# Performance work log

Measured on AMD Instinct MI355X. Metric: run time of the kernel, lower is better.

## Reference

```python
import jax, jax.numpy as jnp
import numpy as np

N_HEAD = 16


def setup_inputs() -> dict:
    key = jax.random.key(0)
    k0, k1, k2, k3 = jax.random.split(key, 4)
    b, n, d = 4, 2048, 1024
    scale = d ** -0.5
    return {
        "x": jax.random.normal(k0, (b, n, d), jnp.float32),
        "Wk": jax.random.normal(k1, (d, d), jnp.float32) * scale,
        "Wq": jax.random.normal(k2, (d, d), jnp.float32) * scale,
        "Wv": jax.random.normal(k3, (d, d), jnp.float32) * scale,
    }


def reference(x, Wk, Wq, Wv):
    b, n, d = x.shape
    hd = d // N_HEAD
    # Linear layers: y = x @ W^T (torch nn.Linear convention), no bias.
    keys = (x @ Wk.T).reshape(b, n, N_HEAD, hd).transpose(0, 2, 1, 3)     # (b,h,n,hd)
    queries = (x @ Wq.T).reshape(b, n, N_HEAD, hd).transpose(0, 2, 1, 3)  # (b,h,n,hd)
    values = (x @ Wv.T).reshape(b, n, N_HEAD, hd).transpose(0, 2, 1, 3)   # computed but UNUSED, as in source
    del values
    # Source does: attn_scores = keys @ queries.transpose(-1,-2)
    # i.e. scores[b,h,i,j] = k_i . q_j ; softmax over j (query axis); no 1/sqrt(d) scaling.
    attn_scores = jnp.einsum("bhid,bhjd->bhij", keys, queries)
    weights = jax.nn.softmax(attn_scores, axis=-1)
    # Source does: weight_scores @ keys (keys, NOT values)
    weighted = jnp.einsum("bhij,bhjd->bhid", weights, keys)  # (b,h,n,hd)
    # Source reshapes (b,h,n,hd) directly to (b,n,h*hd) WITHOUT transposing back.
    return weighted.reshape(b, n, N_HEAD * hd)
```

## Files before the change

### kernel.cpp

```cpp
#include <hip/hip_runtime.h>
#include <cstdint>
#include <cstddef>

#define NTOK 2048
#define DMODEL 1024
#define HD 64
#define MROWS 8192

using f16x8  = __attribute__((ext_vector_type(8))) _Float16;
using f16x4  = __attribute__((ext_vector_type(4))) _Float16;
using f32x4  = __attribute__((ext_vector_type(4))) float;
using f32x16 = __attribute__((ext_vector_type(16))) float;
using u16x8  = __attribute__((ext_vector_type(8))) unsigned short;
using u32x4  = __attribute__((ext_vector_type(4))) unsigned int;

#define Z16 {0.f,0.f,0.f,0.f,0.f,0.f,0.f,0.f,0.f,0.f,0.f,0.f,0.f,0.f,0.f,0.f}

__device__ __forceinline__ unsigned pkf16(float a, float b) {
  return __builtin_bit_cast(unsigned, __builtin_amdgcn_cvt_pkrtz(a, b));
}
__device__ __forceinline__ void plswap(unsigned &a, unsigned &b) {
  auto r = __builtin_amdgcn_permlane32_swap(a, b, false, false);
  a = r[0]; b = r[1];
}
__device__ __forceinline__ float fexp2(float x) {
  return __builtin_amdgcn_exp2f(x);
}

__global__ __launch_bounds__(256) void cvt_f32_f16(const float* __restrict__ in,
                                                   _Float16* __restrict__ out,
                                                   int n4, float scale) {
  int idx = blockIdx.x * 256 + threadIdx.x;
  if (idx < n4) {
    float4 v = reinterpret_cast<const float4*>(in)[idx];
    f16x4 o;
    o.x = (_Float16)(v.x * scale); o.y = (_Float16)(v.y * scale);
    o.z = (_Float16)(v.z * scale); o.w = (_Float16)(v.w * scale);
    reinterpret_cast<f16x4*>(out)[idx] = o;
  }
}

__global__ __launch_bounds__(256) void cvt_w(const float* __restrict__ Wk,
                                             const float* __restrict__ Wq,
                                             _Float16* __restrict__ Wkb,
                                             _Float16* __restrict__ Wqb) {
  const int idx = blockIdx.x * 256 + threadIdx.x;
  const float* in = blockIdx.y ? Wq : Wk;
  _Float16* out = blockIdx.y ? Wqb : Wkb;
  const float scale = blockIdx.y ? 1.4426950408889634f : 1.0f;
  float4 v = reinterpret_cast<const float4*>(in)[idx];
  f16x4 o;
  o.x = (_Float16)(v.x * scale); o.y = (_Float16)(v.y * scale);
  o.z = (_Float16)(v.z * scale); o.w = (_Float16)(v.w * scale);
  reinterpret_cast<f16x4*>(out)[idx] = o;
}

#define GLDS16(g, l) __builtin_amdgcn_global_load_lds(                      \
    (const __attribute__((address_space(1))) void*)(g),                     \
    (__attribute__((address_space(3))) void*)(l), 16, 0, 0)

__global__ __launch_bounds__(256) void gemm_f16(
    const _Float16* __restrict__ X,
    const _Float16* __restrict__ Wk,
    const _Float16* __restrict__ Wq,
    _Float16* __restrict__ Kb,
    _Float16* __restrict__ Qb) {
  const _Float16* __restrict__ W = blockIdx.z ? Wq : Wk;
  _Float16* __restrict__ Y = blockIdx.z ? Qb : Kb;

  __shared__ _Float16 As[2][128 * 32];
  __shared__ _Float16 Bs[2][128 * 32];

  const int tid = threadIdx.x;
  const int lane = tid & 63;
  const int w = tid >> 6;
  const int m0 = blockIdx.x * 128;
  const int o0 = blockIdx.y * 128;

  const int srow = w * 32 + (lane >> 2);
  const int scol = (lane & 3) * 8;
  const _Float16* xsrc = X + (size_t)(m0 + srow) * DMODEL + scol;
  const _Float16* wsrc = W + (size_t)(o0 + srow) * DMODEL + scol;

  const int wr = w >> 1, wc = w & 1;
  const int arow = lane & 15, kg = lane >> 4;

  f32x4 zero = {0.f, 0.f, 0.f, 0.f};
  f32x4 acc[4][4];
#pragma unroll
  for (int mi = 0; mi < 4; ++mi)
#pragma unroll
    for (int ni = 0; ni < 4; ++ni) acc[mi][ni] = zero;

  GLDS16(xsrc,               &As[0][(w * 32) * 32]);
  GLDS16(xsrc + 16 * DMODEL, &As[0][(w * 32 + 16) * 32]);
  GLDS16(wsrc,               &Bs[0][(w * 32) * 32]);
  GLDS16(wsrc + 16 * DMODEL, &Bs[0][(w * 32 + 16) * 32]);

  for (int kt = 0; kt < 32; ++kt) {
    __syncthreads();
    if (kt + 1 < 32) {
      const int ko = (kt + 1) * 32;
      const int bn = (kt + 1) & 1;
      GLDS16(xsrc + ko,               &As[bn][(w * 32) * 32]);
      GLDS16(xsrc + ko + 16 * DMODEL, &As[bn][(w * 32 + 16) * 32]);
      GLDS16(wsrc + ko,               &Bs[bn][(w * 32) * 32]);
      GLDS16(wsrc + ko + 16 * DMODEL, &Bs[bn][(w * 32 + 16) * 32]);
    }
    const int buf = kt & 1;
    f16x8 af[4], bfr[4];
#pragma unroll
    for (int mi = 0; mi < 4; ++mi)
      af[mi] = *reinterpret_cast<const f16x8*>(
          &As[buf][(wr * 64 + mi * 16 + arow) * 32 + kg * 8]);
#pragma unroll
    for (int ni = 0; ni < 4; ++ni)
      bfr[ni] = *reinterpret_cast<const f16x8*>(
          &Bs[buf][(wc * 64 + ni * 16 + arow) * 32 + kg * 8]);
#pragma unroll
    for (int mi = 0; mi < 4; ++mi)
#pragma unroll
      for (int ni = 0; ni < 4; ++ni)
        acc[mi][ni] = __builtin_amdgcn_mfma_f32_16x16x32_f16(
            af[mi], bfr[ni], acc[mi][ni], 0, 0, 0);
  }

#pragma unroll
  for (int mi = 0; mi < 4; ++mi) {
#pragma unroll
    for (int ni = 0; ni < 4; ++ni) {
#pragma unroll
      for (int r = 0; r < 4; ++r) {
        const int m = m0 + wr * 64 + mi * 16 + kg * 4 + r;
        const int o = o0 + wc * 64 + ni * 16 + arow;
        Y[(size_t)m * DMODEL + o] = (_Float16)acc[mi][ni][r];
      }
    }
  }
}

__global__ __launch_bounds__(256) void pack_qkt(
    const _Float16* __restrict__ Qb,
    const _Float16* __restrict__ Kb,
    _Float16* __restrict__ Qp,
    _Float16* __restrict__ KTp) {
  const int blk = blockIdx.x;
  const int bh = blk >> 5;
  const int t64 = blk & 31;
  const int b = bh >> 4, h = bh & 15;
  const int tid = threadIdx.x;
  const _Float16* Src = blockIdx.y ? Kb : Qb;

  __shared__ _Float16 t[64][72];
#pragma unroll
  for (int rr = 0; rr < 2; ++rr) {
    const int c = tid + rr * 256;
    const int jr = c >> 3, dcol = (c & 7) * 8;
    *reinterpret_cast<f16x8*>(&t[jr][dcol]) =
        *reinterpret_cast<const f16x8*>(
            &Src[(size_t)(b * NTOK + t64 * 64 + jr) * DMODEL + h * HD + dcol]);
  }
  __syncthreads();
  if (blockIdx.y == 0) {
#pragma unroll
    for (int rr = 0; rr < 2; ++rr) {
      const int cI = tid + rr * 256;
      const int rs = cI >> 8, ks = (cI >> 6) & 3, l = cI & 63;
      f16x8 v = *reinterpret_cast<const f16x8*>(
          &t[rs * 32 + (l & 31)][ks * 16 + (l >> 5) * 8]);
      const size_t ch = ((size_t)(bh * 64 + t64 * 2 + rs) * 4 + ks) * 512 + l * 8;
      *reinterpret_cast<f16x8*>(&Qp[ch]) = v;
    }
  } else {
#pragma unroll
    for (int rr = 0; rr < 2; ++rr) {
      const int cI = tid + rr * 256;
      const int ds = cI >> 8, ks = (cI >> 6) & 3, l = cI & 63;
      const int col = ds * 32 + (l & 31);
      const int row0 = ks * 16 + (l >> 5) * 8;
      f16x8 v;
#pragma unroll
      for (int e = 0; e < 8; ++e) v[e] = t[row0 + e][col];
      const size_t ch = (((size_t)(bh * 32 + t64) * 2 + ds) * 4 + ks) * 512 + l * 8;
      *reinterpret_cast<f16x8*>(&KTp[ch]) = v;
    }
  }
}

__global__ __launch_bounds__(256) void attn_mfma(
    const _Float16* __restrict__ Kb,
    const _Float16* __restrict__ Qp,
    const _Float16* __restrict__ KTp,
    float* __restrict__ out) {
  const int bid = blockIdx.x;
  const int myid = (bid & 7) * 128 + (bid >> 3);
  const int bh = myid >> 4;
  const int itile = myid & 15;
  const int b = bh >> 4, h = bh & 15;
  const int tid = threadIdx.x, lane = tid & 63, w = tid >> 6;
  const int l31 = lane & 31;
  const int hi = lane >> 5;
  const int hi8 = hi * 8;
  const int i0 = itile * 128 + w * 32;

  const _Float16* Kh   = Kb + (size_t)b * NTOK * DMODEL + h * HD;
  const _Float16* qpp  = Qp  + (size_t)bh * 131072 + lane * 8;
  const _Float16* ktpp = KTp + (size_t)bh * 131072 + lane * 8;

  __shared__ float lsl[4][32];
  __shared__ float scl[4][32];

  f16x8 kbf[4];
#pragma unroll
  for (int ks = 0; ks < 4; ++ks)
    kbf[ks] = *reinterpret_cast<const f16x8*>(
        &Kh[(size_t)(i0 + l31) * DMODEL + ks * 16 + hi8]);

  const f32x16 z16v = Z16;
  f32x16 o0 = z16v, o1 = z16v;
  float mreg = -1e30f, ls = 0.f;

  f16x8 qA0[4], qA1[4], qB0[4], qB1[4];
  f32x16 sA0, sA1, sB0, sB1;

#define LOADQ(QD0, QD1, JT)                                                   \
  _Pragma("unroll")                                                           \
  for (int ks = 0; ks < 4; ++ks) {                                            \
    QD0[ks] = *reinterpret_cast<const f16x8*>(                                \
        qpp + ((size_t)(JT) * 8 + ks) * 512);                                 \
    QD1[ks] = *reinterpret_cast<const f16x8*>(                                \
        qpp + ((size_t)(JT) * 8 + 4 + ks) * 512);                             \
  }

#define QK_TILE(SD0, SD1, Q0, Q1)                                             \
  SD0 = z16v; SD1 = z16v;                                                     \
  __builtin_amdgcn_s_setprio(1);                                              \
  _Pragma("unroll")                                                           \
  for (int ks = 0; ks < 4; ++ks) {                                            \
    SD0 = __builtin_amdgcn_mfma_f32_32x32x16_f16(Q0[ks], kbf[ks], SD0, 0,0,0);\
    SD1 = __builtin_amdgcn_mfma_f32_32x32x16_f16(Q1[ks], kbf[ks], SD1, 0,0,0);\
  }                                                                           \
  __builtin_amdgcn_s_setprio(0);

#define SMPV_TILE(S0, S1, JT)                                                 \
  {                                                                           \
          \
    f16x8 kt0[4], kt1[4];                                                     \
    _Pragma("unroll")                                                         \
    for (int ks = 0; ks < 4; ++ks) {                                          \
      kt0[ks] = *reinterpret_cast<const f16x8*>(                              \
          ktpp + ((size_t)(JT) * 8 + ks) * 512);                              \
      kt1[ks] = *reinterpret_cast<const f16x8*>(                              \
          ktpp + ((size_t)(JT) * 8 + 4 + ks) * 512);                          \
    }                                                                         \
    float m0 = fmaxf(S0[0], S1[0]);                                           \
    float m1 = fmaxf(S0[1], S1[1]);                                           \
    float m2 = fmaxf(S0[2], S1[2]);                                           \
    float m3 = fmaxf(S0[3], S1[3]);                                           \
    _Pragma("unroll")                                                         \
    for (int r = 4; r < 16; r += 4) {                                         \
      m0 = fmaxf(m0, fmaxf(S0[r], S1[r]));                                    \
      m1 = fmaxf(m1, fmaxf(S0[r + 1], S1[r + 1]));                            \
      m2 = fmaxf(m2, fmaxf(S0[r + 2], S1[r + 2]));                            \
      m3 = fmaxf(m3, fmaxf(S0[r + 3], S1[r + 3]));                            \
    }                                                                         \
    float pm = fmaxf(fmaxf(m0, m1), fmaxf(m2, m3));                           \
    pm = fmaxf(pm, __shfl_xor(pm, 32));                                       \
    if (!__all(pm <= mreg + 8.0f)) {                                          \
      const float mn = fmaxf(mreg, pm);                                       \
      const float sc = fexp2(mreg - mn);                                      \
      ls *= sc;                                                               \
      mreg = mn;                                                              \
      scl[w][l31] = sc;                                                       \
      _Pragma("unroll")                                                       \
      for (int r = 0; r < 16; ++r) {                                          \
        const int il = (r & 3) + 8 * (r >> 2) + 4 * hi;                       \
        const float scr = scl[w][il];                                         \
        o0[r] *= scr; o1[r] *= scr;                                           \
      }                                                                       \
    }                                                                         \
    float p0a[16], p1a[16];                                                   \
    _Pragma("unroll")                                                         \
    for (int r = 0; r < 16; ++r) {                                            \
      p0a[r] = fexp2(S0[r] - mreg);                                           \
      p1a[r] = fexp2(S1[r] - mreg);                                           \
    }                                                                         \
    float l0 = 0.f, l1 = 0.f, l2 = 0.f, l3 = 0.f;                             \
    _Pragma("unroll")                                                         \
    for (int r = 0; r < 16; r += 4) {                                         \
      l0 += p0a[r]     + p1a[r];                                              \
      l1 += p0a[r + 1] + p1a[r + 1];                                          \
      l2 += p0a[r + 2] + p1a[r + 2];                                          \
      l3 += p0a[r + 3] + p1a[r + 3];                                          \
    }                                                                         \
    ls += (l0 + l1) + (l2 + l3);                                              \
    f16x8 pfr[4];                                                             \
    {                                                                         \
      unsigned a0 = pkf16(p0a[0], p0a[1]),  b0 = pkf16(p0a[4], p0a[5]);       \
      unsigned a1 = pkf16(p0a[2], p0a[3]),  b1 = pkf16(p0a[6], p0a[7]);       \
      plswap(a0, b0); plswap(a1, b1);                                         \
      u32x4 t; t[0] = a0; t[1] = a1; t[2] = b0; t[3] = b1;                    \
      pfr[0] = __builtin_bit_cast(f16x8, t);                                  \
      unsigned a2 = pkf16(p0a[8], p0a[9]),   b2 = pkf16(p0a[12], p0a[13]);    \
      unsigned a3 = pkf16(p0a[10], p0a[11]), b3 = pkf16(p0a[14], p0a[15]);    \
      plswap(a2, b2); plswap(a3, b3);                                         \
      t[0] = a2; t[1] = a3; t[2] = b2; t[3] = b3;                             \
      pfr[1] = __builtin_bit_cast(f16x8, t);                                  \
      unsigned a4 = pkf16(p1a[0], p1a[1]),  b4 = pkf16(p1a[4], p1a[5]);       \
      unsigned a5 = pkf16(p1a[2], p1a[3]),  b5 = pkf16(p1a[6], p1a[7]);       \
      plswap(a4, b4); plswap(a5, b5);                                         \
      t[0] = a4; t[1] = a5; t[2] = b4; t[3] = b5;                             \
      pfr[2] = __builtin_bit_cast(f16x8, t);                                  \
      unsigned a6 = pkf16(p1a[8], p1a[9]),   b6 = pkf16(p1a[12], p1a[13]);    \
      unsigned a7 = pkf16(p1a[10], p1a[11]), b7 = pkf16(p1a[14], p1a[15]);    \
      plswap(a6, b6); plswap(a7, b7);                                         \
      t[0] = a6; t[1] = a7; t[2] = b6; t[3] = b7;                             \
      pfr[3] = __builtin_bit_cast(f16x8, t);                                  \
    }                                                                         \
    __builtin_amdgcn_s_setprio(1);                                            \
    _Pragma("unroll")                                                         \
    for (int ks = 0; ks < 4; ++ks) {                                          \
      o0 = __builtin_amdgcn_mfma_f32_32x32x16_f16(pfr[ks], kt0[ks], o0, 0,0,0);\
      o1 = __builtin_amdgcn_mfma_f32_32x32x16_f16(pfr[ks], kt1[ks], o1, 0,0,0);\
    }                                                                         \
    __builtin_amdgcn_s_setprio(0);                                            \
  }

  LOADQ(qA0, qA1, 0)
  QK_TILE(sA0, sA1, qA0, qA1)
  LOADQ(qB0, qB1, 1)

  for (int jt = 0; jt < 30; jt += 2) {
    QK_TILE(sB0, sB1, qB0, qB1)
    LOADQ(qA0, qA1, jt + 2)
    SMPV_TILE(sA0, sA1, jt)
    QK_TILE(sA0, sA1, qA0, qA1)
    LOADQ(qB0, qB1, jt + 3)
    SMPV_TILE(sB0, sB1, jt + 1)
  }
  QK_TILE(sB0, sB1, qB0, qB1)
  SMPV_TILE(sA0, sA1, 30)
  SMPV_TILE(sB0, sB1, 31)

#undef LOADQ
#undef QK_TILE
#undef SMPV_TILE

  lsl[w][l31] = ls + __shfl_xor(ls, 32);
  __syncthreads();
#pragma unroll
  for (int r = 0; r < 16; ++r) {
    const int il = (r & 3) + 8 * (r >> 2) + 4 * hi;
    const float inv = 1.0f / lsl[w][il];
    const size_t rowb = ((size_t)bh * NTOK + i0 + il) * HD;
    out[rowb + l31]      = o0[r] * inv;
    out[rowb + 32 + l31] = o1[r] * inv;
  }
}

extern "C" void kernel_launch(void* const* d_in, const int* in_sizes, int n_in,
                              void* d_out, int out_size, void* d_ws, size_t ws_size,
                              hipStream_t stream) {
  const float* x  = (const float*)d_in[0];
  const float* Wk = (const float*)d_in[1];
  const float* Wq = (const float*)d_in[2];
  float* out = (float*)d_out;

  _Float16* xb  = (_Float16*)d_ws;
  _Float16* Qp  = xb;
  _Float16* Wkb = xb + (size_t)8388608;
  _Float16* Wqb = Wkb + (size_t)1048576;
  _Float16* Kb  = Wqb + (size_t)1048576;
  _Float16* Qb  = Kb + (size_t)8388608;
  _Float16* KTp = Qb;

  cvt_f32_f16<<<8192, 256, 0, stream>>>(x, xb, 2097152, 1.0f);
  cvt_w<<<dim3(1024, 2), 256, 0, stream>>>(Wk, Wq, Wkb, Wqb);

  dim3 ggrid(MROWS / 128, DMODEL / 128, 2);
  gemm_f16<<<ggrid, 256, 0, stream>>>(xb, Wkb, Wqb, Kb, Qb);

  pack_qkt<<<dim3(2048, 2), 256, 0, stream>>>(Qb, Kb, Qp, KTp);

  attn_mfma<<<1024, 256, 0, stream>>>(Kb, Qp, KTp, out);
}
```

Before: 187.1 us.

## Process 64 key rows per wave to reuse Q and K^T fragment loads

Each wave now handles two 32-row key blocks (64 rows), so each loaded Q and K^T fragment feeds twice as many MFMAs. The key tile per j-step shrinks to 32 columns, iterated 64 times, and the grid is halved to 512 blocks. The explicit two-stage software pipeline of QK and softmax/PV is dropped for a plain loop, and the __syncthreads before the final normalization is removed. The aim is to cut global/L2 load traffic per MFMA, at the cost of more registers, fewer blocks (lower occupancy) and less latency hiding.

```diff
diff --git a/kernel.cpp b/kernel.cpp
--- a/kernel.cpp
+++ b/kernel.cpp
@@ -193,168 +193,144 @@
     const _Float16* __restrict__ KTp,
     float* __restrict__ out) {
   const int bid = blockIdx.x;
-  const int myid = (bid & 7) * 128 + (bid >> 3);
-  const int bh = myid >> 4;
-  const int itile = myid & 15;
+  const int myid = (bid & 7) * 64 + (bid >> 3);
+  const int bh = myid >> 3;
+  const int itile = myid & 7;
   const int b = bh >> 4, h = bh & 15;
   const int tid = threadIdx.x, lane = tid & 63, w = tid >> 6;
   const int l31 = lane & 31;
   const int hi = lane >> 5;
   const int hi8 = hi * 8;
-  const int i0 = itile * 128 + w * 32;
+  const int i0 = itile * 256 + w * 64;
 
   const _Float16* Kh   = Kb + (size_t)b * NTOK * DMODEL + h * HD;
   const _Float16* qpp  = Qp  + (size_t)bh * 131072 + lane * 8;
   const _Float16* ktpp = KTp + (size_t)bh * 131072 + lane * 8;
 
-  __shared__ float lsl[4][32];
-  __shared__ float scl[4][32];
-
-  f16x8 kbf[4];
-#pragma unroll
-  for (int ks = 0; ks < 4; ++ks)
-    kbf[ks] = *reinterpret_cast<const f16x8*>(
+  __shared__ float lsl[4][2][32];
+  __shared__ float scl[4][2][32];
+
+  f16x8 kbf0[4], kbf1[4];
+#pragma unroll
+  for (int ks = 0; ks < 4; ++ks) {
+    kbf0[ks] = *reinterpret_cast<const f16x8*>(
         &Kh[(size_t)(i0 + l31) * DMODEL + ks * 16 + hi8]);
+    kbf1[ks] = *reinterpret_cast<const f16x8*>(
+        &Kh[(size_t)(i0 + 32 + l31) * DMODEL + ks * 16 + hi8]);
+  }
 
   const f32x16 z16v = Z16;
-  f32x16 o0 = z16v, o1 = z16v;
-  float mreg = -1e30f, ls = 0.f;
-
-  f16x8 qA0[4], qA1[4], qB0[4], qB1[4];
-  f32x16 sA0, sA1, sB0, sB1;
-
-#define LOADQ(QD0, QD1, JT)                                                   \
-  _Pragma("unroll")                                                           \
-  for (int ks = 0; ks < 4; ++ks) {                                            \
-    QD0[ks] = *reinterpret_cast<const f16x8*>(                                \
-        qpp + ((size_t)(JT) * 8 + ks) * 512);                                 \
-    QD1[ks] = *reinterpret_cast<const f16x8*>(                                \
-        qpp + ((size_t)(JT) * 8 + 4 + ks) * 512);                             \
-  }
-
-#define QK_TILE(SD0, SD1, Q0, Q1)                                             \
-  SD0 = z16v; SD1 = z16v;                                                     \
-  __builtin_amdgcn_s_setprio(1);                                              \
-  _Pragma("unroll")                                                           \
-  for (int ks = 0; ks < 4; ++ks) {                                            \
-    SD0 = __builtin_amdgcn_mfma_f32_32x32x16_f16(Q0[ks], kbf[ks], SD0, 0,0,0);\
-    SD1 = __builtin_amdgcn_mfma_f32_32x32x16_f16(Q1[ks], kbf[ks], SD1, 0,0,0);\
-  }                                                                           \
-  __builtin_amdgcn_s_setprio(0);
-
-#define SMPV_TILE(S0, S1, JT)                                                 \
-  {                                                                           \
-          \
-    f16x8 kt0[4], kt1[4];                                                     \
-    _Pragma("unroll")                                                         \
-    for (int ks = 0; ks < 4; ++ks) {                                          \
-      kt0[ks] = *reinterpret_cast<const f16x8*>(                              \
-          ktpp + ((size_t)(JT) * 8 + ks) * 512);                              \
-      kt1[ks] = *reinterpret_cast<const f16x8*>(                              \
-          ktpp + ((size_t)(JT) * 8 + 4 + ks) * 512);                          \
-    }                                                                         \
-    float m0 = fmaxf(S0[0], S1[0]);                                           \
-    float m1 = fmaxf(S0[1], S1[1]);                                           \
-    float m2 = fmaxf(S0[2], S1[2]);                                           \
-    float m3 = fmaxf(S0[3], S1[3]);                                           \
-    _Pragma("unroll")                                                         \
-    for (int r = 4; r < 16; r += 4) {                                         \
-      m0 = fmaxf(m0, fmaxf(S0[r], S1[r]));                                    \
-      m1 = fmaxf(m1, fmaxf(S0[r + 1], S1[r + 1]));                            \
-      m2 = fmaxf(m2, fmaxf(S0[r + 2], S1[r + 2]));                            \
-      m3 = fmaxf(m3, fmaxf(S0[r + 3], S1[r + 3]));                            \
-    }                                                                         \
-    float pm = fmaxf(fmaxf(m0, m1), fmaxf(m2, m3));                           \
-    pm = fmaxf(pm, __shfl_xor(pm, 32));                                       \
-    if (!__all(pm <= mreg + 8.0f)) {                                          \
-      const float mn = fmaxf(mreg, pm);                                       \
-      const float sc = fexp2(mreg - mn);                                      \
-      ls *= sc;                                                               \
-      mreg = mn;                                                              \
-      scl[w][l31] = sc;                                                       \
+  f32x16 o00 = z16v, o01 = z16v, o10 = z16v, o11 = z16v;
+  float m0reg = -1e30f, ls0 = 0.f;
+  float m1reg = -1e30f, ls1 = 0.f;
+
+  for (int jt = 0; jt < 64; ++jt) {
+    f16x8 q[4];
+#pragma unroll
+    for (int ks = 0; ks < 4; ++ks)
+      q[ks] = *reinterpret_cast<const f16x8*>(qpp + ((size_t)jt * 4 + ks) * 512);
+
+    f32x16 s0 = z16v, s1 = z16v;
+    __builtin_amdgcn_s_setprio(1);
+#pragma unroll
+    for (int ks = 0; ks < 4; ++ks)
+      s0 = __builtin_amdgcn_mfma_f32_32x32x16_f16(q[ks], kbf0[ks], s0, 0, 0, 0);
+#pragma unroll
+    for (int ks = 0; ks < 4; ++ks)
+      s1 = __builtin_amdgcn_mfma_f32_32x32x16_f16(q[ks], kbf1[ks], s1, 0, 0, 0);
+    __builtin_amdgcn_s_setprio(0);
+
+    f16x8 kt0[2], kt1[2];
+    {
+      const size_t base = ((size_t)(jt >> 1) * 8 + (jt & 1) * 2) * 512;
+#pragma unroll
+      for (int kk = 0; kk < 2; ++kk) {
+        kt0[kk] = *reinterpret_cast<const f16x8*>(ktpp + base + (size_t)kk * 512);
+        kt1[kk] = *reinterpret_cast<const f16x8*>(ktpp + base + (size_t)(4 + kk) * 512);
+      }
+    }
+
+    f16x8 pfr0[2], pfr1[2];
+
+#define SOFTMAX_BLOCK(S, MREG, LS, SCL, PFR)                                  \
+    {                                                                         \
+      float m0 = fmaxf(S[0], S[4]);                                           \
+      float m1 = fmaxf(S[1], S[5]);                                           \
+      float m2 = fmaxf(S[2], S[6]);                                           \
+      float m3 = fmaxf(S[3], S[7]);                                           \
       _Pragma("unroll")                                                       \
-      for (int r = 0; r < 16; ++r) {                                          \
-        const int il = (r & 3) + 8 * (r >> 2) + 4 * hi;                       \
-        const float scr = scl[w][il];                                         \
-        o0[r] *= scr; o1[r] *= scr;                                           \
+      for (int r = 8; r < 16; r += 4) {                                       \
+        m0 = fmaxf(m0, S[r]);                                                 \
+        m1 = fmaxf(m1, S[r + 1]);                                             \
+        m2 = fmaxf(m2, S[r + 2]);                                             \
+        m3 = fmaxf(m3, S[r + 3]);                                             \
       }                                                                       \
-    }                                                                         \
-    float p0a[16], p1a[16];                                                   \
-    _Pragma("unroll")                                                         \
-    for (int r = 0; r < 16; ++r) {                                            \
-      p0a[r] = fexp2(S0[r] - mreg);                                           \
-      p1a[r] = fexp2(S1[r] - mreg);                                           \
-    }                                                                         \
-    float l0 = 0.f, l1 = 0.f, l2 = 0.f, l3 = 0.f;                             \
-    _Pragma("unroll")                                                         \
-    for (int r = 0; r < 16; r += 4) {                                         \
-      l0 += p0a[r]     + p1a[r];                                              \
-      l1 += p0a[r + 1] + p1a[r + 1];                                          \
-      l2 += p0a[r + 2] + p1a[r + 2];                                          \
-      l3 += p0a[r + 3] + p1a[r + 3];                                          \
-    }                                                                         \
-    ls += (l0 + l1) + (l2 + l3);                                              \
-    f16x8 pfr[4];                                                             \
-    {                                                                         \
-      unsigned a0 = pkf16(p0a[0], p0a[1]),  b0 = pkf16(p0a[4], p0a[5]);       \
-      unsigned a1 = pkf16(p0a[2], p0a[3]),  b1 = pkf16(p0a[6], p0a[7]);       \
+      float pm = fmaxf(fmaxf(m0, m1), fmaxf(m2, m3));                         \
+      pm = fmaxf(pm, __shfl_xor(pm, 32));                                     \
+      if (!__all(pm <= MREG + 8.0f)) {                                        \
+        const float mn = fmaxf(MREG, pm);                                     \
+        const float sc = fexp2(MREG - mn);                                    \
+        LS *= sc;                                                             \
+        MREG = mn;                                                            \
+        SCL[l31] = sc;                                                        \
+        _Pragma("unroll")                                                     \
+        for (int r = 0; r < 16; ++r) {                                        \
+          const int il = (r & 3) + 8 * (r >> 2) + 4 * hi;                     \
+          const float scr = SCL[il];                                          \
+          if (&S == &s0) { o00[r] *= scr; o01[r] *= scr; }                    \
+          else           { o10[r] *= scr; o11[r] *= scr; }                    \
+        }                                                                     \
+      }                                                                       \
+      float pa[16];                                                           \
+      _Pragma("unroll")                                                       \
+      for (int r = 0; r < 16; ++r) pa[r] = fexp2(S[r] - MREG);                \
+      float l0 = 0.f, l1 = 0.f, l2 = 0.f, l3 = 0.f;                           \
+      _Pragma("unroll")                                                       \
+      for (int r = 0; r < 16; r += 4) {                                       \
+        l0 += pa[r];     l1 += pa[r + 1];                                     \
+        l2 += pa[r + 2]; l3 += pa[r + 3];                                     \
+      }                                                                       \
+      LS += (l0 + l1) + (l2 + l3);                                            \
+      unsigned a0 = pkf16(pa[0], pa[1]),  b0 = pkf16(pa[4], pa[5]);           \
+      unsigned a1 = pkf16(pa[2], pa[3]),  b1 = pkf16(pa[6], pa[7]);           \
       plswap(a0, b0); plswap(a1, b1);                                         \
       u32x4 t; t[0] = a0; t[1] = a1; t[2] = b0; t[3] = b1;                    \
-      pfr[0] = __builtin_bit_cast(f16x8, t);                                  \
-      unsigned a2 = pkf16(p0a[8], p0a[9]),   b2 = pkf16(p0a[12], p0a[13]);    \
-      unsigned a3 = pkf16(p0a[10], p0a[11]), b3 = pkf16(p0a[14], p0a[15]);    \
+      PFR[0] = __builtin_bit_cast(f16x8, t);                                  \
+      unsigned a2 = pkf16(pa[8], pa[9]),   b2 = pkf16(pa[12], pa[13]);        \
+      unsigned a3 = pkf16(pa[10], pa[11]), b3 = pkf16(pa[14], pa[15]);        \
       plswap(a2, b2); plswap(a3, b3);                                         \
       t[0] = a2; t[1] = a3; t[2] = b2; t[3] = b3;                             \
-      pfr[1] = __builtin_bit_cast(f16x8, t);                                  \
-      unsigned a4 = pkf16(p1a[0], p1a[1]),  b4 = pkf16(p1a[4], p1a[5]);       \
-      unsigned a5 = pkf16(p1a[2], p1a[3]),  b5 = pkf16(p1a[6], p1a[7]);       \
-      plswap(a4, b4); plswap(a5, b5);                                         \
-      t[0] = a4; t[1] = a5; t[2] = b4; t[3] = b5;                             \
-      pfr[2] = __builtin_bit_cast(f16x8, t);                                  \
-      unsigned a6 = pkf16(p1a[8], p1a[9]),   b6 = pkf16(p1a[12], p1a[13]);    \
-      unsigned a7 = pkf16(p1a[10], p1a[11]), b7 = pkf16(p1a[14], p1a[15]);    \
-      plswap(a6, b6); plswap(a7, b7);                                         \
-      t[0] = a6; t[1] = a7; t[2] = b6; t[3] = b7;                             \
-      pfr[3] = __builtin_bit_cast(f16x8, t);                                  \
-    }                                                                         \
-    __builtin_amdgcn_s_setprio(1);                                            \
-    _Pragma("unroll")                                                         \
-    for (int ks = 0; ks < 4; ++ks) {                                          \
-      o0 = __builtin_amdgcn_mfma_f32_32x32x16_f16(pfr[ks], kt0[ks], o0, 0,0,0);\
-      o1 = __builtin_amdgcn_mfma_f32_32x32x16_f16(pfr[ks], kt1[ks], o1, 0,0,0);\
-    }                                                                         \
-    __builtin_amdgcn_s_setprio(0);                                            \
-  }
-
-  LOADQ(qA0, qA1, 0)
-  QK_TILE(sA0, sA1, qA0, qA1)
-  LOADQ(qB0, qB1, 1)
-
-  for (int jt = 0; jt < 30; jt += 2) {
-    QK_TILE(sB0, sB1, qB0, qB1)
-    LOADQ(qA0, qA1, jt + 2)
-    SMPV_TILE(sA0, sA1, jt)
-    QK_TILE(sA0, sA1, qA0, qA1)
-    LOADQ(qB0, qB1, jt + 3)
-    SMPV_TILE(sB0, sB1, jt + 1)
-  }
-  QK_TILE(sB0, sB1, qB0, qB1)
-  SMPV_TILE(sA0, sA1, 30)
-  SMPV_TILE(sB0, sB1, 31)
-
-#undef LOADQ
-#undef QK_TILE
-#undef SMPV_TILE
-
-  lsl[w][l31] = ls + __shfl_xor(ls, 32);
-  __syncthreads();
+      PFR[1] = __builtin_bit_cast(f16x8, t);                                  \
+    }
+
+    SOFTMAX_BLOCK(s0, m0reg, ls0, scl[w][0], pfr0)
+    SOFTMAX_BLOCK(s1, m1reg, ls1, scl[w][1], pfr1)
+#undef SOFTMAX_BLOCK
+
+    __builtin_amdgcn_s_setprio(1);
+#pragma unroll
+    for (int kk = 0; kk < 2; ++kk) {
+      o00 = __builtin_amdgcn_mfma_f32_32x32x16_f16(pfr0[kk], kt0[kk], o00, 0, 0, 0);
+      o01 = __builtin_amdgcn_mfma_f32_32x32x16_f16(pfr0[kk], kt1[kk], o01, 0, 0, 0);
+      o10 = __builtin_amdgcn_mfma_f32_32x32x16_f16(pfr1[kk], kt0[kk], o10, 0, 0, 0);
+      o11 = __builtin_amdgcn_mfma_f32_32x32x16_f16(pfr1[kk], kt1[kk], o11, 0, 0, 0);
+    }
+    __builtin_amdgcn_s_setprio(0);
+  }
+
+  lsl[w][0][l31] = ls0 + __shfl_xor(ls0, 32);
+  lsl[w][1][l31] = ls1 + __shfl_xor(ls1, 32);
 #pragma unroll
   for (int r = 0; r < 16; ++r) {
     const int il = (r & 3) + 8 * (r >> 2) + 4 * hi;
-    const float inv = 1.0f / lsl[w][il];
-    const size_t rowb = ((size_t)bh * NTOK + i0 + il) * HD;
-    out[rowb + l31]      = o0[r] * inv;
-    out[rowb + 32 + l31] = o1[r] * inv;
+    const float inv0 = 1.0f / lsl[w][0][il];
+    const float inv1 = 1.0f / lsl[w][1][il];
+    const size_t rowb0 = ((size_t)bh * NTOK + i0 + il) * HD;
+    const size_t rowb1 = ((size_t)bh * NTOK + i0 + 32 + il) * HD;
+    out[rowb0 + l31]      = o00[r] * inv0;
+    out[rowb0 + 32 + l31] = o01[r] * inv0;
+    out[rowb1 + l31]      = o10[r] * inv1;
+    out[rowb1 + 32 + l31] = o11[r] * inv1;
   }
 }
 
@@ -382,5 +358,5 @@
 
   pack_qkt<<<dim3(2048, 2), 256, 0, stream>>>(Qb, Kb, Qp, KTp);
 
-  attn_mfma<<<1024, 256, 0, stream>>>(Kb, Qp, KTp, out);
-}
+  attn_mfma<<<512, 256, 0, stream>>>(Kb, Qp, KTp, out);
+}
```

Result: slower. 210.8 us (+12.6%).
